# Optimization experiments

Measured on AMD Instinct MI355X. Metric: run time of the kernel, lower is better.

The kernel has to match this reference:

```python
import jax, jax.numpy as jnp
import numpy as np

B, H, W, DIM = 64, 28, 28, 384
N = B * H * W
E, K, R = 3, 2, 8
HID = 4 * DIM
SCALING = 8.0 / 8.0  # alpha / r


def setup_inputs() -> dict:
    key = jax.random.key(0)
    ks = jax.random.split(key, 8)
    x = jax.random.normal(ks[0], (B, H, W, DIM), dtype=jnp.float32)
    gate = jax.random.uniform(ks[1], (N, E), dtype=jnp.float32)
    topk_probs = jax.random.uniform(ks[2], (N, K), dtype=jnp.float32)
    topk_idx = jax.random.randint(ks[3], (N, K), 0, E)
    # LoRA expert params (w_up is zeros in the original init; use small randn
    # so the MoE path is numerically non-trivial for kernel testing)
    w_down = jax.random.normal(ks[4], (E, DIM, R), dtype=jnp.float32) * (1.0 / DIM ** 0.5)
    w_up = jax.random.normal(ks[5], (E, R, DIM), dtype=jnp.float32) * 0.02
    # frozen base ConvNeXt MLP: Linear(dim,4dim) -> GELU -> Linear(4dim,dim)
    W1 = jax.random.normal(ks[6], (DIM, HID), dtype=jnp.float32) * 0.02
    b1 = jnp.zeros((HID,), dtype=jnp.float32)
    W2 = jax.random.normal(ks[7], (HID, DIM), dtype=jnp.float32) * 0.02
    b2 = jnp.zeros((DIM,), dtype=jnp.float32)
    return {"x": x, "gate": gate, "topk_probs": topk_probs, "topk_idx": topk_idx,
            "w_down": w_down, "w_up": w_up, "W1": W1, "b1": b1, "W2": W2, "b2": b2}


def reference(x, gate, topk_probs, topk_idx, w_down, w_up, W1, b1, W2, b2):
    gelu = lambda t: jax.nn.gelu(t, approximate=False)  # torch nn.GELU() default = exact erf
    # frozen base MLP
    orig = gelu(jnp.einsum('bhwd,df->bhwf', x, W1) + b1)
    orig = jnp.einsum('bhwf,fd->bhwd', orig, W2) + b2
    # MoE LoRA path over flattened tokens
    x_flat = x.reshape(-1, x.shape[-1])          # [N, dim]
    moe = jnp.zeros_like(x_flat)
    n_experts = w_down.shape[0]
    for i in range(n_experts):
        # combined routing weight for expert i (0 for tokens not routed here)
        prob = jnp.sum(jnp.where(topk_idx == i, topk_probs, 0.0), axis=1)  # [N]
        out_i = gelu(x_flat @ w_down[i]) @ w_up[i] * SCALING               # [N, dim]
        moe = moe + out_i * prob[:, None]
    return orig + moe.reshape(x.shape)
```

## Files before the change

kernel.cpp:

```cpp
#include <hip/hip_runtime.h>
#include <hip/hip_bf16.h>

typedef __attribute__((ext_vector_type(4))) float float4v;
typedef __attribute__((ext_vector_type(8))) __bf16 bf16x8;
typedef __attribute__((ext_vector_type(8))) unsigned short ushort8v;

constexpr int NTOK = 50176;
constexpr int DIM  = 384;
constexpr int HID  = 1536;
constexpr int BM   = 128;
constexpr int NTH  = 512;
constexpr int NBLK = NTOK / BM;
constexpr int NCH  = 24;

constexpr int IMG_WD  = 0;
constexpr int IMG_WUP = 24576;
constexpr int IMG_W1  = 49152;
constexpr int IMG_W2  = 49152 + 24*49152;
constexpr size_t WS_NEED = 2408448;
constexpr int NELEMS = 1204224;

constexpr int L_X  = 0;
constexpr int L_W  = 98304;
constexpr int L_HS = 147456;
constexpr int LDSZ = 163840;

__device__ __forceinline__ unsigned short f2bf(float f) {
  __hip_bfloat16 h = __float2bfloat16(f);
  return *reinterpret_cast<unsigned short*>(&h);
}

__device__ __forceinline__ float gelu_f(float v) {
  float u = 0.7978845608f * (v + 0.044715f * v * v * v);
  float e = __expf(2.0f * u);
  float t = 1.0f - 2.0f / (e + 1.0f);
  return 0.5f * v * (1.0f + t);
}

__device__ __forceinline__ void stage_load(const char* src, int tid, ushort8v st[6]) {
  #pragma unroll
  for (int j = 0; j < 6; ++j)
    st[j] = *(const ushort8v*)(src + tid * 16 + j * 8192);
}
__device__ __forceinline__ void stage_write(char* dst, int tid, const ushort8v st[6]) {
  #pragma unroll
  for (int j = 0; j < 6; ++j)
    *(ushort8v*)(dst + tid * 16 + j * 8192) = st[j];
}

__global__ __launch_bounds__(256) void pack_k(
    const float* __restrict__ W1, const float* __restrict__ W2,
    const float* __restrict__ wd, const float* __restrict__ wu,
    unsigned short* __restrict__ img)
{
  int i = blockIdx.x * 256 + threadIdx.x;
  if (i >= NELEMS) return;
  if (i < 12288) {
    int r = i / 384; int inb = (i % 384) * 2;
    int d = (inb ^ ((r & 7) << 4)) >> 1;
    float f = (r < 24) ? wd[(r >> 3) * (DIM * 8) + d * 8 + (r & 7)] : 0.f;
    img[i] = f2bf(f);
  } else if (i < 24576) {
    int j = i - 12288; int a = j * 2;
    int dh = a >> 7; int b6 = (a >> 6) & 1;
    int d = dh * 2 + (b6 ^ ((dh >> 1) & 1));
    int k = ((a & 63) ^ ((d & 3) << 4)) >> 1;
    float f = (k < 24) ? wu[k * DIM + d] : 0.f;
    img[i] = f2bf(f);
  } else if (i < 24576 + 589824) {
    int j = i - 24576; int h = j / 24576; int jc = j % 24576;
    int r = jc / 384; int inb = (jc % 384) * 2;
    int d = (inb ^ ((r & 7) << 4)) >> 1;
    img[i] = f2bf(W1[d * HID + h * 64 + r]);
  } else {
    int j = i - 24576 - 589824; int h = j / 24576; int jc = j % 24576;
    int dd = jc / 64; int inb = (jc % 64) * 2;
    int k2 = (inb ^ ((dd & 7) << 4)) >> 1;
    img[i] = f2bf(W2[(h * 64 + k2) * DIM + dd]);
  }
}

__global__ __launch_bounds__(NTH, 2) void fused_k(
    const float* __restrict__ x,
    const float* __restrict__ tp,
    const int*   __restrict__ ti,
    const float* __restrict__ b1,
    const float* __restrict__ b2,
    const unsigned short* __restrict__ img,
    float* __restrict__ out)
{
  extern __shared__ char lds[];
  const int tid = threadIdx.x, wid = tid >> 6, lane = tid & 63;
  const int lrow = lane & 15, g4 = lane >> 4, lkb = g4 * 8;
  const int blockRow = blockIdx.x * BM;
  const char* imgc = (const char*)img;

  ushort8v st[6];

  stage_load(imgc + IMG_WD, tid, st);
  {
    const float* xb = x + (size_t)blockRow * DIM;
    #pragma unroll
    for (int it = 0; it < 12; ++it) {
      int idx = it * NTH + tid;
      int row = idx / 48, c8 = idx % 48;
      float4v v0 = *(const float4v*)(xb + row * DIM + c8 * 8);
      float4v v1 = *(const float4v*)(xb + row * DIM + c8 * 8 + 4);
      ushort8v u;
      u[0]=f2bf(v0[0]); u[1]=f2bf(v0[1]); u[2]=f2bf(v0[2]); u[3]=f2bf(v0[3]);
      u[4]=f2bf(v1[0]); u[5]=f2bf(v1[1]); u[6]=f2bf(v1[2]); u[7]=f2bf(v1[3]);
      int byte = (row * 768 + c8 * 16) ^ ((row & 7) << 4);
      *(ushort8v*)(lds + L_X + byte) = u;
    }
  }
  __syncthreads();
  stage_write(lds + L_W, tid, st);
  __syncthreads();
  stage_load(imgc + IMG_W1, tid, st);

  const int band = wid >> 1, chh = wid & 1;
  float4v h2[2] = {};
  {
    int rbw = chh * 16 + lrow, sww = (rbw & 7) << 4;
    int ra0 = band * 32 + lrow, ra1 = ra0 + 16;
    int s0 = (ra0 & 7) << 4, s1 = (ra1 & 7) << 4;
    #pragma unroll
    for (int ks = 0; ks < 12; ++ks) {
      int ko = (ks * 32 + lkb) * 2;
      bf16x8 a0 = *(const bf16x8*)(lds + L_X + ((ra0 * 768 + ko) ^ s0));
      bf16x8 a1 = *(const bf16x8*)(lds + L_X + ((ra1 * 768 + ko) ^ s1));
      bf16x8 b  = *(const bf16x8*)(lds + L_W + ((rbw * 768 + ko) ^ sww));
      h2[0] = __builtin_amdgcn_mfma_f32_16x16x32_bf16(a0, b, h2[0], 0, 0, 0);
      h2[1] = __builtin_amdgcn_mfma_f32_16x16x32_bf16(a1, b, h2[1], 0, 0, 0);
    }
  }
  {
    int col = chh * 16 + lrow; int e = col >> 3;
    #pragma unroll
    for (int mt = 0; mt < 2; ++mt) {
      #pragma unroll
      for (int r = 0; r < 4; ++r) {
        int row = band * 32 + mt * 16 + g4 * 4 + r;
        int token = blockRow + row;
        float p = 0.f;
        if (e < 3) {
          int i0 = ti[token * 2], i1 = ti[token * 2 + 1];
          if (i0 == e) p += tp[token * 2];
          if (i1 == e) p += tp[token * 2 + 1];
        }
        float gv = p * gelu_f(h2[mt][r]);
        int byte = (row * 128 + col * 2) ^ ((row & 7) << 4);
        *(unsigned short*)(lds + L_HS + byte) = f2bf(gv);
      }
    }
  }
  __syncthreads();

  const int wr = wid >> 2, wc = wid & 3;
  float4v acc[4][6] = {};
  {
    bf16x8 A[4];
    #pragma unroll
    for (int mt = 0; mt < 4; ++mt) {
      int ra = wr * 64 + mt * 16 + lrow;
      A[mt] = *(const bf16x8*)(lds + L_HS + ((ra * 128 + lkb * 2) ^ ((ra & 7) << 4)));
    }
    #pragma unroll
    for (int nt = 0; nt < 6; ++nt) {
      int rb = wc * 96 + nt * 16 + lrow;
      bf16x8 b = *(const bf16x8*)(lds + L_W + 24576 + ((rb * 64 + lkb * 2) ^ ((rb & 7) << 4)));
      #pragma unroll
      for (int mt = 0; mt < 4; ++mt)
        acc[mt][nt] = __builtin_amdgcn_mfma_f32_16x16x32_bf16(A[mt], b, acc[mt][nt], 0, 0, 0);
    }
  }

  for (int h = 0; h < NCH; ++h) {
    __syncthreads();
    stage_write(lds + L_W, tid, st);
    __syncthreads();
    stage_load(imgc + IMG_W2 + h * 49152, tid, st);

    float4v hv[2][2] = {};
    {
      int ra0 = band * 32 + lrow, ra1 = ra0 + 16;
      int s0 = (ra0 & 7) << 4, s1 = (ra1 & 7) << 4;
      int rb0 = chh * 32 + lrow, rb1 = rb0 + 16;
      int t0 = (rb0 & 7) << 4, t1 = (rb1 & 7) << 4;
      #pragma unroll
      for (int ks = 0; ks < 12; ++ks) {
        int ko = (ks * 32 + lkb) * 2;
        bf16x8 a0 = *(const bf16x8*)(lds + L_X + ((ra0 * 768 + ko) ^ s0));
        bf16x8 a1 = *(const bf16x8*)(lds + L_X + ((ra1 * 768 + ko) ^ s1));
        bf16x8 b0 = *(const bf16x8*)(lds + L_W + ((rb0 * 768 + ko) ^ t0));
        bf16x8 b1v= *(const bf16x8*)(lds + L_W + ((rb1 * 768 + ko) ^ t1));
        hv[0][0] = __builtin_amdgcn_mfma_f32_16x16x32_bf16(a0, b0,  hv[0][0], 0, 0, 0);
        hv[0][1] = __builtin_amdgcn_mfma_f32_16x16x32_bf16(a0, b1v, hv[0][1], 0, 0, 0);
        hv[1][0] = __builtin_amdgcn_mfma_f32_16x16x32_bf16(a1, b0,  hv[1][0], 0, 0, 0);
        hv[1][1] = __builtin_amdgcn_mfma_f32_16x16x32_bf16(a1, b1v, hv[1][1], 0, 0, 0);
      }
    }
    #pragma unroll
    for (int nt = 0; nt < 2; ++nt) {
      int col = chh * 32 + nt * 16 + lrow;
      float bb = b1[h * 64 + col];
      #pragma unroll
      for (int mt = 0; mt < 2; ++mt) {
        #pragma unroll
        for (int r = 0; r < 4; ++r) {
          int row = band * 32 + mt * 16 + g4 * 4 + r;
          float gv = gelu_f(hv[mt][nt][r] + bb);
          int byte = (row * 128 + col * 2) ^ ((row & 7) << 4);
          *(unsigned short*)(lds + L_HS + byte) = f2bf(gv);
        }
      }
    }
    __syncthreads();
    stage_write(lds + L_W, tid, st);
    __syncthreads();
    if (h < NCH - 1)
      stage_load(imgc + IMG_W1 + (h + 1) * 49152, tid, st);

    #pragma unroll
    for (int kk = 0; kk < 2; ++kk) {
      int kb = kk * 32 + lkb;
      bf16x8 A[4];
      #pragma unroll
      for (int mt = 0; mt < 4; ++mt) {
        int ra = wr * 64 + mt * 16 + lrow;
        A[mt] = *(const bf16x8*)(lds + L_HS + ((ra * 128 + kb * 2) ^ ((ra & 7) << 4)));
      }
      #pragma unroll
      for (int nt = 0; nt < 6; ++nt) {
        int rb = wc * 96 + nt * 16 + lrow;
        bf16x8 b = *(const bf16x8*)(lds + L_W + ((rb * 128 + kb * 2) ^ ((rb & 7) << 4)));
        #pragma unroll
        for (int mt = 0; mt < 4; ++mt)
          acc[mt][nt] = __builtin_amdgcn_mfma_f32_16x16x32_bf16(A[mt], b, acc[mt][nt], 0, 0, 0);
      }
    }
  }

  #pragma unroll
  for (int nt = 0; nt < 6; ++nt) {
    int col = wc * 96 + nt * 16 + lrow;
    float bb = b2[col];
    #pragma unroll
    for (int mt = 0; mt < 4; ++mt) {
      #pragma unroll
      for (int r = 0; r < 4; ++r) {
        int row = wr * 64 + mt * 16 + g4 * 4 + r;
        out[(size_t)(blockRow + row) * DIM + col] = acc[mt][nt][r] + bb;
      }
    }
  }
}

extern "C" void kernel_launch(void* const* d_in, const int* in_sizes, int n_in,
                              void* d_out, int out_size, void* d_ws, size_t ws_size,
                              hipStream_t stream) {
  const float* x          = (const float*)d_in[0];
  const float* topk_probs = (const float*)d_in[2];
  const int*   topk_idx   = (const int*)  d_in[3];
  const float* w_down     = (const float*)d_in[4];
  const float* w_up       = (const float*)d_in[5];
  const float* W1         = (const float*)d_in[6];
  const float* b1         = (const float*)d_in[7];
  const float* W2         = (const float*)d_in[8];
  const float* b2         = (const float*)d_in[9];
  float* out = (float*)d_out;

  if (ws_size < WS_NEED) return;

  hipFuncSetAttribute(reinterpret_cast<const void*>(fused_k),
                      hipFuncAttributeMaxDynamicSharedMemorySize, LDSZ);

  unsigned short* img = (unsigned short*)d_ws;
  pack_k<<<(NELEMS + 255) / 256, 256, 0, stream>>>(W1, W2, w_down, w_up, img);
  fused_k<<<NBLK, NTH, LDSZ, stream>>>(x, topk_probs, topk_idx, b1, b2, img, out);
}
```

Measured before the change: 306.1 us.

## Halve token tile and keep x fragments in registers instead of LDS

Halves the token tile per block from 128 to 64 and loads each wave's x fragments once into registers (12 bf16x8) instead of holding the whole x tile in shared memory. This cuts LDS use from about 160KB to about 56KB and raises the launch-bounds occupancy hint from 2 to 4 blocks. The aim is more resident blocks to hide weight staging and sync latency. In exchange, each block streams the full W1/W2 weights for half as many tokens, doubling global weight traffic, and register pressure may cause spills at the higher occupancy target.

```diff
diff --git a/kernel.cpp b/kernel.cpp
--- a/kernel.cpp
+++ b/kernel.cpp
@@ -8,7 +8,7 @@
 constexpr int NTOK = 50176;
 constexpr int DIM  = 384;
 constexpr int HID  = 1536;
-constexpr int BM   = 128;
+constexpr int BM   = 64;
 constexpr int NTH  = 512;
 constexpr int NBLK = NTOK / BM;
 constexpr int NCH  = 24;
@@ -20,10 +20,9 @@
 constexpr size_t WS_NEED = 2408448;
 constexpr int NELEMS = 1204224;
 
-constexpr int L_X  = 0;
-constexpr int L_W  = 98304;
-constexpr int L_HS = 147456;
-constexpr int LDSZ = 163840;
+constexpr int L_W  = 0;
+constexpr int L_HS = 49152;
+constexpr int LDSZ = 57344;
 
 __device__ __forceinline__ unsigned short f2bf(float f) {
   __hip_bfloat16 h = __float2bfloat16(f);
@@ -80,7 +79,7 @@
   }
 }
 
-__global__ __launch_bounds__(NTH, 2) void fused_k(
+__global__ __launch_bounds__(NTH, 4) void fused_k(
     const float* __restrict__ x,
     const float* __restrict__ tp,
     const int*   __restrict__ ti,
@@ -101,7 +100,7 @@
   {
     const float* xb = x + (size_t)blockRow * DIM;
     #pragma unroll
-    for (int it = 0; it < 12; ++it) {
+    for (int it = 0; it < 6; ++it) {
       int idx = it * NTH + tid;
       int row = idx / 48, c8 = idx % 48;
       float4v v0 = *(const float4v*)(xb + row * DIM + c8 * 8);
@@ -110,59 +109,61 @@
       u[0]=f2bf(v0[0]); u[1]=f2bf(v0[1]); u[2]=f2bf(v0[2]); u[3]=f2bf(v0[3]);
       u[4]=f2bf(v1[0]); u[5]=f2bf(v1[1]); u[6]=f2bf(v1[2]); u[7]=f2bf(v1[3]);
       int byte = (row * 768 + c8 * 16) ^ ((row & 7) << 4);
-      *(ushort8v*)(lds + L_X + byte) = u;
-    }
-  }
-  __syncthreads();
+      *(ushort8v*)(lds + L_W + byte) = u;
+    }
+  }
+  __syncthreads();
+
+  const int band = wid >> 1, chh = wid & 1;
+  bf16x8 xf[12];
+  {
+    int row = band * 16 + lrow;
+    int rb = row * 768, sw = (row & 7) << 4;
+    #pragma unroll
+    for (int ks = 0; ks < 12; ++ks)
+      xf[ks] = *(const bf16x8*)(lds + L_W + ((rb + (ks * 32 + lkb) * 2) ^ sw));
+  }
+  __syncthreads();
+
   stage_write(lds + L_W, tid, st);
-  __syncthreads();
   stage_load(imgc + IMG_W1, tid, st);
-
-  const int band = wid >> 1, chh = wid & 1;
-  float4v h2[2] = {};
+  __syncthreads();
+
+  float4v h2 = {};
   {
     int rbw = chh * 16 + lrow, sww = (rbw & 7) << 4;
-    int ra0 = band * 32 + lrow, ra1 = ra0 + 16;
-    int s0 = (ra0 & 7) << 4, s1 = (ra1 & 7) << 4;
     #pragma unroll
     for (int ks = 0; ks < 12; ++ks) {
-      int ko = (ks * 32 + lkb) * 2;
-      bf16x8 a0 = *(const bf16x8*)(lds + L_X + ((ra0 * 768 + ko) ^ s0));
-      bf16x8 a1 = *(const bf16x8*)(lds + L_X + ((ra1 * 768 + ko) ^ s1));
-      bf16x8 b  = *(const bf16x8*)(lds + L_W + ((rbw * 768 + ko) ^ sww));
-      h2[0] = __builtin_amdgcn_mfma_f32_16x16x32_bf16(a0, b, h2[0], 0, 0, 0);
-      h2[1] = __builtin_amdgcn_mfma_f32_16x16x32_bf16(a1, b, h2[1], 0, 0, 0);
+      bf16x8 b = *(const bf16x8*)(lds + L_W + ((rbw * 768 + (ks * 32 + lkb) * 2) ^ sww));
+      h2 = __builtin_amdgcn_mfma_f32_16x16x32_bf16(xf[ks], b, h2, 0, 0, 0);
     }
   }
   {
     int col = chh * 16 + lrow; int e = col >> 3;
     #pragma unroll
+    for (int r = 0; r < 4; ++r) {
+      int row = band * 16 + g4 * 4 + r;
+      int token = blockRow + row;
+      float p = 0.f;
+      if (e < 3) {
+        int i0 = ti[token * 2], i1 = ti[token * 2 + 1];
+        if (i0 == e) p += tp[token * 2];
+        if (i1 == e) p += tp[token * 2 + 1];
+      }
+      float gv = p * gelu_f(h2[r]);
+      int byte = (row * 128 + col * 2) ^ ((row & 7) << 4);
+      *(unsigned short*)(lds + L_HS + byte) = f2bf(gv);
+    }
+  }
+  __syncthreads();
+
+  const int wr = wid >> 2, wc = wid & 3;
+  float4v acc[2][6] = {};
+  {
+    bf16x8 A[2];
+    #pragma unroll
     for (int mt = 0; mt < 2; ++mt) {
-      #pragma unroll
-      for (int r = 0; r < 4; ++r) {
-        int row = band * 32 + mt * 16 + g4 * 4 + r;
-        int token = blockRow + row;
-        float p = 0.f;
-        if (e < 3) {
-          int i0 = ti[token * 2], i1 = ti[token * 2 + 1];
-          if (i0 == e) p += tp[token * 2];
-          if (i1 == e) p += tp[token * 2 + 1];
-        }
-        float gv = p * gelu_f(h2[mt][r]);
-        int byte = (row * 128 + col * 2) ^ ((row & 7) << 4);
-        *(unsigned short*)(lds + L_HS + byte) = f2bf(gv);
-      }
-    }
-  }
-  __syncthreads();
-
-  const int wr = wid >> 2, wc = wid & 3;
-  float4v acc[4][6] = {};
-  {
-    bf16x8 A[4];
-    #pragma unroll
-    for (int mt = 0; mt < 4; ++mt) {
-      int ra = wr * 64 + mt * 16 + lrow;
+      int ra = wr * 32 + mt * 16 + lrow;
       A[mt] = *(const bf16x8*)(lds + L_HS + ((ra * 128 + lkb * 2) ^ ((ra & 7) << 4)));
     }
     #pragma unroll
@@ -170,7 +171,7 @@
       int rb = wc * 96 + nt * 16 + lrow;
       bf16x8 b = *(const bf16x8*)(lds + L_W + 24576 + ((rb * 64 + lkb * 2) ^ ((rb & 7) << 4)));
       #pragma unroll
-      for (int mt = 0; mt < 4; ++mt)
+      for (int mt = 0; mt < 2; ++mt)
         acc[mt][nt] = __builtin_amdgcn_mfma_f32_16x16x32_bf16(A[mt], b, acc[mt][nt], 0, 0, 0);
     }
   }
@@ -181,23 +182,17 @@
     __syncthreads();
     stage_load(imgc + IMG_W2 + h * 49152, tid, st);
 
-    float4v hv[2][2] = {};
+    float4v hv[2] = {};
     {
-      int ra0 = band * 32 + lrow, ra1 = ra0 + 16;
-      int s0 = (ra0 & 7) << 4, s1 = (ra1 & 7) << 4;
       int rb0 = chh * 32 + lrow, rb1 = rb0 + 16;
       int t0 = (rb0 & 7) << 4, t1 = (rb1 & 7) << 4;
       #pragma unroll
       for (int ks = 0; ks < 12; ++ks) {
         int ko = (ks * 32 + lkb) * 2;
-        bf16x8 a0 = *(const bf16x8*)(lds + L_X + ((ra0 * 768 + ko) ^ s0));
-        bf16x8 a1 = *(const bf16x8*)(lds + L_X + ((ra1 * 768 + ko) ^ s1));
         bf16x8 b0 = *(const bf16x8*)(lds + L_W + ((rb0 * 768 + ko) ^ t0));
         bf16x8 b1v= *(const bf16x8*)(lds + L_W + ((rb1 * 768 + ko) ^ t1));
-        hv[0][0] = __builtin_amdgcn_mfma_f32_16x16x32_bf16(a0, b0,  hv[0][0], 0, 0, 0);
-        hv[0][1] = __builtin_amdgcn_mfma_f32_16x16x32_bf16(a0, b1v, hv[0][1], 0, 0, 0);
-        hv[1][0] = __builtin_amdgcn_mfma_f32_16x16x32_bf16(a1, b0,  hv[1][0], 0, 0, 0);
-        hv[1][1] = __builtin_amdgcn_mfma_f32_16x16x32_bf16(a1, b1v, hv[1][1], 0, 0, 0);
+        hv[0] = __builtin_amdgcn_mfma_f32_16x16x32_bf16(xf[ks], b0,  hv[0], 0, 0, 0);
+        hv[1] = __builtin_amdgcn_mfma_f32_16x16x32_bf16(xf[ks], b1v, hv[1], 0, 0, 0);
       }
     }
     #pragma unroll
@@ -205,14 +200,11 @@
       int col = chh * 32 + nt * 16 + lrow;
       float bb = b1[h * 64 + col];
       #pragma unroll
-      for (int mt = 0; mt < 2; ++mt) {
-        #pragma unroll
-        for (int r = 0; r < 4; ++r) {
-          int row = band * 32 + mt * 16 + g4 * 4 + r;
-          float gv = gelu_f(hv[mt][nt][r] + bb);
-          int byte = (row * 128 + col * 2) ^ ((row & 7) << 4);
-          *(unsigned short*)(lds + L_HS + byte) = f2bf(gv);
-        }
+      for (int r = 0; r < 4; ++r) {
+        int row = band * 16 + g4 * 4 + r;
+        float gv = gelu_f(hv[nt][r] + bb);
+        int byte = (row * 128 + col * 2) ^ ((row & 7) << 4);
+        *(unsigned short*)(lds + L_HS + byte) = f2bf(gv);
       }
     }
     __syncthreads();
@@ -224,10 +216,10 @@
     #pragma unroll
     for (int kk = 0; kk < 2; ++kk) {
       int kb = kk * 32 + lkb;
-      bf16x8 A[4];
-      #pragma unroll
-      for (int mt = 0; mt < 4; ++mt) {
-        int ra = wr * 64 + mt * 16 + lrow;
+      bf16x8 A[2];
+      #pragma unroll
+      for (int mt = 0; mt < 2; ++mt) {
+        int ra = wr * 32 + mt * 16 + lrow;
         A[mt] = *(const bf16x8*)(lds + L_HS + ((ra * 128 + kb * 2) ^ ((ra & 7) << 4)));
       }
       #pragma unroll
@@ -235,7 +227,7 @@
         int rb = wc * 96 + nt * 16 + lrow;
         bf16x8 b = *(const bf16x8*)(lds + L_W + ((rb * 128 + kb * 2) ^ ((rb & 7) << 4)));
         #pragma unroll
-        for (int mt = 0; mt < 4; ++mt)
+        for (int mt = 0; mt < 2; ++mt)
           acc[mt][nt] = __builtin_amdgcn_mfma_f32_16x16x32_bf16(A[mt], b, acc[mt][nt], 0, 0, 0);
       }
     }
@@ -246,10 +238,10 @@
     int col = wc * 96 + nt * 16 + lrow;
     float bb = b2[col];
     #pragma unroll
-    for (int mt = 0; mt < 4; ++mt) {
+    for (int mt = 0; mt < 2; ++mt) {
       #pragma unroll
       for (int r = 0; r < 4; ++r) {
-        int row = wr * 64 + mt * 16 + g4 * 4 + r;
+        int row = wr * 32 + mt * 16 + g4 * 4 + r;
         out[(size_t)(blockRow + row) * DIM + col] = acc[mt][nt][r] + bb;
       }
     }
```

New measurement: 833.3 us. +172.2%, slower.
